# Optimization experiments

Hardware: AMD Instinct MI355X
Metric: run time of the kernel (lower is better)

Reference implementation:

```python
import jax, jax.numpy as jnp
import numpy as np

N, FEAT, H, D, E, C = 3072, 512, 8, 8, 100000, 2
ALPHA = 0.2  # LeakyReLU slope
NEG_INF = -9e15


def setup_inputs() -> dict:
    key = jax.random.key(0)
    ks = jax.random.split(key, 12)
    x = jax.random.normal(ks[0], (N, FEAT), dtype=jnp.float32)
    adj = (jax.random.uniform(ks[1], (N, N)) < 0.002).astype(jnp.float32)
    adj = jnp.maximum(adj, jnp.eye(N, dtype=jnp.float32))
    L = jax.random.randint(ks[2], (E,), 0, N)
    R = jax.random.randint(ks[3], (E,), 0, N)
    label = jax.random.randint(ks[4], (E,), 0, C)
    s = 1.0 / np.sqrt(FEAT)
    W = jax.random.uniform(ks[5], (H, FEAT, D), minval=-s, maxval=s, dtype=jnp.float32)
    sa = 1.0 / np.sqrt(2 * D)
    a1 = jax.random.uniform(ks[6], (H, D), minval=-sa, maxval=sa, dtype=jnp.float32)
    a2 = jax.random.uniform(ks[7], (H, D), minval=-sa, maxval=sa, dtype=jnp.float32)
    s1 = 1.0 / np.sqrt(H * D * 2)
    W1 = jax.random.uniform(ks[8], (H * D * 2, 64), minval=-s1, maxval=s1, dtype=jnp.float32)
    b1 = jnp.zeros((64,), dtype=jnp.float32)
    s2 = 1.0 / np.sqrt(64)
    W2 = jax.random.uniform(ks[9], (64, C), minval=-s2, maxval=s2, dtype=jnp.float32)
    b2 = jnp.zeros((C,), dtype=jnp.float32)
    return {"x": x, "adj": adj, "L": L, "R": R, "label": label,
            "W": W, "a1": a1, "a2": a2, "W1": W1, "b1": b1, "W2": W2, "b2": b2}


def _encoder(x, adj, W, a1, a2):
    # Wh: [H, N, D]
    Wh = jnp.einsum('nf,hfd->hnd', x, W)
    # broadcast attention logits: e[h,i,j] = leaky_relu(Wh_i.a1 + Wh_j.a2)
    s1 = jnp.einsum('hnd,hd->hn', Wh, a1)[:, :, None]   # [H,N,1]
    s2 = jnp.einsum('hnd,hd->hn', Wh, a2)[:, None, :]   # [H,1,N]
    e = jax.nn.leaky_relu(s1 + s2, negative_slope=ALPHA)  # [H,N,N]
    e = jnp.where(adj[None] > 0, e, NEG_INF)
    att = jax.nn.softmax(e, axis=-1)                      # [H,N,N]
    h = jnp.einsum('hnm,hmd->hnd', att, Wh)               # [H,N,D]
    h = jax.nn.elu(h)                                     # concat=True -> ELU
    # concat heads: [N, H*D]
    return jnp.transpose(h, (1, 0, 2)).reshape(x.shape[0], -1)


def reference(x, adj, L, R, label, W, a1, a2, W1, b1, W2, b2):
    emb = _encoder(x, adj, W, a1, a2)            # [N, 64]
    lr = jnp.concatenate([emb[L], emb[R]], axis=1)  # [E, 128]
    hcls = jax.nn.relu(lr @ W1 + b1)
    logits = hcls @ W2 + b2                       # [E, C]
    logp = jax.nn.log_softmax(logits, axis=-1)
    nll = -jnp.take_along_axis(logp, label[:, None], axis=1)[:, 0]
    return jnp.mean(nll)
```

## Files before the change

kernel.cpp:

```cpp
#include <hip/hip_runtime.h>
#include <math.h>

#define NN 3072
#define FEAT 512
#define HD 64
#define NE 100000
#define ALPHA 0.2f
#define CAP 96
#define CAPP 97
#define AROWS 8
#define K5_BLOCKS 2048

__global__ __launch_bounds__(256) void k_stage1(const float* __restrict__ adj, const float* __restrict__ x,
                                                const float* __restrict__ W, const float* __restrict__ a1,
                                                const float* __restrict__ a2, int* __restrict__ nbr,
                                                int* __restrict__ cnt, float* __restrict__ Wh,
                                                float* __restrict__ s1t, float* __restrict__ s2t) {
    __shared__ float xs4t[FEAT][4];
    __shared__ float part[4][4][HD];
    int b = blockIdx.x;
    int tid = threadIdx.x;
    int wid = tid >> 6, lane = tid & 63;

    if (b & 1) {
        int i = (b >> 1) * 4 + wid;
        const float4* row = (const float4*)&adj[(size_t)i * NN];
        float4 v[12];
        #pragma unroll
        for (int c = 0; c < 12; ++c) v[c] = row[c * 64 + lane];
        unsigned long long lmask = (1ull << lane) - 1ull;
        int base = 0;
        #pragma unroll
        for (int c = 0; c < 12; ++c) {
            #pragma unroll
            for (int k = 0; k < 4; ++k) {
                float vk = k == 0 ? v[c].x : k == 1 ? v[c].y : k == 2 ? v[c].z : v[c].w;
                bool nz = vk > 0.f;
                unsigned long long m = __ballot(nz);
                if (nz) {
                    int pos = base + __popcll(m & lmask);
                    if (pos < CAP) nbr[i * CAP + pos] = c * 256 + lane * 4 + k;
                }
                base += __popcll(m);
            }
        }
        if (lane == 0) cnt[i] = base < CAP ? base : CAP;
    } else {
        int n0 = (b >> 1) * 4;
        for (int idx = tid; idx < 512; idx += 256) {
            int r = idx >> 7, fq = idx & 127;
            float4 xv = ((const float4*)x)[(size_t)(n0 + r) * (FEAT / 4) + fq];
            xs4t[fq * 4 + 0][r] = xv.x;
            xs4t[fq * 4 + 1][r] = xv.y;
            xs4t[fq * 4 + 2][r] = xv.z;
            xs4t[fq * 4 + 3][r] = xv.w;
        }
        __syncthreads();
        int fsub = lane >> 4, h = (lane >> 1) & 7, dq = lane & 1;
        const float4* W4 = (const float4*)W;
        int base4 = h * 1024 + dq;
        int f0 = wid * (FEAT / 4);
        float4 acc0 = {0.f,0.f,0.f,0.f}, acc1 = acc0, acc2 = acc0, acc3 = acc0;
        #pragma unroll 8
        for (int f4 = 0; f4 < 32; ++f4) {
            int f = f0 + f4 * 4 + fsub;
            float4 w4 = W4[base4 + f * 2];
            float4 xv = *(const float4*)&xs4t[f][0];
            acc0.x = fmaf(xv.x, w4.x, acc0.x); acc0.y = fmaf(xv.x, w4.y, acc0.y);
            acc0.z = fmaf(xv.x, w4.z, acc0.z); acc0.w = fmaf(xv.x, w4.w, acc0.w);
            acc1.x = fmaf(xv.y, w4.x, acc1.x); acc1.y = fmaf(xv.y, w4.y, acc1.y);
            acc1.z = fmaf(xv.y, w4.z, acc1.z); acc1.w = fmaf(xv.y, w4.w, acc1.w);
            acc2.x = fmaf(xv.z, w4.x, acc2.x); acc2.y = fmaf(xv.z, w4.y, acc2.y);
            acc2.z = fmaf(xv.z, w4.z, acc2.z); acc2.w = fmaf(xv.z, w4.w, acc2.w);
            acc3.x = fmaf(xv.w, w4.x, acc3.x); acc3.y = fmaf(xv.w, w4.y, acc3.y);
            acc3.z = fmaf(xv.w, w4.z, acc3.z); acc3.w = fmaf(xv.w, w4.w, acc3.w);
        }
        #define RED4(A) \
            A.x += __shfl_xor(A.x, 16, 64); A.x += __shfl_xor(A.x, 32, 64); \
            A.y += __shfl_xor(A.y, 16, 64); A.y += __shfl_xor(A.y, 32, 64); \
            A.z += __shfl_xor(A.z, 16, 64); A.z += __shfl_xor(A.z, 32, 64); \
            A.w += __shfl_xor(A.w, 16, 64); A.w += __shfl_xor(A.w, 32, 64);
        RED4(acc0) RED4(acc1) RED4(acc2) RED4(acc3)
        #undef RED4
        if (fsub == 0) {
            int o = h * 8 + dq * 4;
            *(float4*)&part[wid][0][o] = acc0;
            *(float4*)&part[wid][1][o] = acc1;
            *(float4*)&part[wid][2][o] = acc2;
            *(float4*)&part[wid][3][o] = acc3;
        }
        __syncthreads();
        int n = n0 + wid;
        float v = part[0][wid][lane] + part[1][wid][lane] + part[2][wid][lane] + part[3][wid][lane];
        Wh[n * HD + lane] = v;
        float t1 = v * a1[lane];
        float t2 = v * a2[lane];
        for (int m = 1; m < 8; m <<= 1) {
            t1 += __shfl_xor(t1, m, 64);
            t2 += __shfl_xor(t2, m, 64);
        }
        if ((lane & 7) == 0) {
            int h2 = lane >> 3;
            s1t[n * 8 + h2] = t1;
            s2t[n * 8 + h2] = t2;
        }
    }
}

__global__ __launch_bounds__(512) void k_attn_pq(const float* __restrict__ Wh, const float* __restrict__ s1t,
                                                 const float* __restrict__ s2t, const int* __restrict__ nbr,
                                                 const int* __restrict__ cnt, const float* __restrict__ W1,
                                                 const float* __restrict__ b1, float* __restrict__ P,
                                                 float* __restrict__ Q) {
    __shared__ float W1s[2 * HD][HD];
    __shared__ int   jbuf[AROWS][CAP];
    __shared__ float ebuf[AROWS][8][CAPP];
    __shared__ float es[AROWS][HD];
    int tid = threadIdx.x;
    int wid = tid >> 6;
    int lane = tid & 63;
    int i = blockIdx.x * AROWS + wid;
    int h = lane >> 3, d = lane & 7;
    int ni = cnt[i];
    float s1i = s1t[i * 8 + h];
    for (int k = lane; k < CAP; k += 64)
        if (k < ni) jbuf[wid][k] = nbr[i * CAP + k];
    for (int idx = tid; idx < 2048; idx += 512)
        ((float4*)W1s)[idx] = ((const float4*)W1)[idx];
    __syncthreads();
    float mloc = -INFINITY;
    for (int k = d; k < ni; k += 8) {
        int j = jbuf[wid][k];
        float ev = s1i + s2t[j * 8 + h];
        ev = ev > 0.f ? ev : ALPHA * ev;
        ebuf[wid][h][k] = ev;
        mloc = fmaxf(mloc, ev);
    }
    mloc = fmaxf(mloc, __shfl_xor(mloc, 1, 8));
    mloc = fmaxf(mloc, __shfl_xor(mloc, 2, 8));
    mloc = fmaxf(mloc, __shfl_xor(mloc, 4, 8));
    __syncthreads();
    float denom = 0.f, acc = 0.f;
    for (int k = 0; k < ni; ++k) {
        float p = __expf(ebuf[wid][h][k] - mloc);
        denom += p;
        acc = fmaf(p, Wh[jbuf[wid][k] * HD + lane], acc);
    }
    float o = acc / denom;
    o = o > 0.f ? o : expm1f(o);
    es[wid][lane] = o;
    __syncthreads();
    float p = b1[lane], q = 0.f;
    #pragma unroll 8
    for (int k = 0; k < HD; ++k) {
        float e = es[wid][k];
        p = fmaf(e, W1s[k][lane], p);
        q = fmaf(e, W1s[HD + k][lane], q);
    }
    P[i * HD + lane] = p;
    Q[i * HD + lane] = q;
}

__global__ __launch_bounds__(256) void k_cls(const float* __restrict__ P, const float* __restrict__ Q,
                                             const int* __restrict__ L, const int* __restrict__ R,
                                             const int* __restrict__ label, const float* __restrict__ W2,
                                             const float* __restrict__ b2, float* __restrict__ partials) {
    int tid = threadIdx.x;
    int sl = tid & 15;
    int g = (blockIdx.x * 256 + tid) >> 4;
    float2 wa = *(const float2*)&W2[(sl * 4 + 0) * 2];
    float2 wb = *(const float2*)&W2[(sl * 4 + 1) * 2];
    float2 wc = *(const float2*)&W2[(sl * 4 + 2) * 2];
    float2 wd = *(const float2*)&W2[(sl * 4 + 3) * 2];
    float b20 = b2[0], b21 = b2[1];

    int e0 = g, e1 = g + 32768, e2 = g + 65536;
    int ln0 = L[e0], rn0 = R[e0], lb0 = label[e0];
    int ln1 = L[e1], rn1 = R[e1], lb1 = label[e1];
    int ln2 = L[e2], rn2 = R[e2], lb2 = label[e2];
    float4 p0 = *(const float4*)&P[ln0 * HD + sl * 4];
    float4 q0 = *(const float4*)&Q[rn0 * HD + sl * 4];
    float4 p1 = *(const float4*)&P[ln1 * HD + sl * 4];
    float4 q1 = *(const float4*)&Q[rn1 * HD + sl * 4];
    float4 p2 = *(const float4*)&P[ln2 * HD + sl * 4];
    float4 q2 = *(const float4*)&Q[rn2 * HD + sl * 4];

    float v00 = fmaxf(p0.x + q0.x, 0.f), v01 = fmaxf(p0.y + q0.y, 0.f);
    float v02 = fmaxf(p0.z + q0.z, 0.f), v03 = fmaxf(p0.w + q0.w, 0.f);
    float v10 = fmaxf(p1.x + q1.x, 0.f), v11 = fmaxf(p1.y + q1.y, 0.f);
    float v12 = fmaxf(p1.z + q1.z, 0.f), v13 = fmaxf(p1.w + q1.w, 0.f);
    float v20 = fmaxf(p2.x + q2.x, 0.f), v21 = fmaxf(p2.y + q2.y, 0.f);
    float v22 = fmaxf(p2.z + q2.z, 0.f), v23 = fmaxf(p2.w + q2.w, 0.f);

    float t00 = v00 * wa.x + v01 * wb.x + v02 * wc.x + v03 * wd.x;
    float t01 = v00 * wa.y + v01 * wb.y + v02 * wc.y + v03 * wd.y;
    float t10 = v10 * wa.x + v11 * wb.x + v12 * wc.x + v13 * wd.x;
    float t11 = v10 * wa.y + v11 * wb.y + v12 * wc.y + v13 * wd.y;
    float t20 = v20 * wa.x + v21 * wb.x + v22 * wc.x + v23 * wd.x;
    float t21 = v20 * wa.y + v21 * wb.y + v22 * wc.y + v23 * wd.y;
    #pragma unroll
    for (int m = 1; m < 16; m <<= 1) {
        t00 += __shfl_xor(t00, m, 64);  t01 += __shfl_xor(t01, m, 64);
        t10 += __shfl_xor(t10, m, 64);  t11 += __shfl_xor(t11, m, 64);
        t20 += __shfl_xor(t20, m, 64);  t21 += __shfl_xor(t21, m, 64);
    }
    float sum;
    {
        float l0 = t00 + b20, l1 = t01 + b21;
        float mx = fmaxf(l0, l1);
        sum = mx + __logf(__expf(l0 - mx) + __expf(l1 - mx)) - (lb0 ? l1 : l0);
        l0 = t10 + b20; l1 = t11 + b21; mx = fmaxf(l0, l1);
        sum += mx + __logf(__expf(l0 - mx) + __expf(l1 - mx)) - (lb1 ? l1 : l0);
        l0 = t20 + b20; l1 = t21 + b21; mx = fmaxf(l0, l1);
        sum += mx + __logf(__expf(l0 - mx) + __expf(l1 - mx)) - (lb2 ? l1 : l0);
    }
    if (g + 98304 < NE) {
        int e3 = g + 98304;
        int ln3 = L[e3], rn3 = R[e3], lb3 = label[e3];
        float4 p3 = *(const float4*)&P[ln3 * HD + sl * 4];
        float4 q3 = *(const float4*)&Q[rn3 * HD + sl * 4];
        float w0 = fmaxf(p3.x + q3.x, 0.f), w1 = fmaxf(p3.y + q3.y, 0.f);
        float w2 = fmaxf(p3.z + q3.z, 0.f), w3 = fmaxf(p3.w + q3.w, 0.f);
        float t30 = w0 * wa.x + w1 * wb.x + w2 * wc.x + w3 * wd.x;
        float t31 = w0 * wa.y + w1 * wb.y + w2 * wc.y + w3 * wd.y;
        #pragma unroll
        for (int m = 1; m < 16; m <<= 1) {
            t30 += __shfl_xor(t30, m, 64);  t31 += __shfl_xor(t31, m, 64);
        }
        float l0 = t30 + b20, l1 = t31 + b21;
        float mx = fmaxf(l0, l1);
        sum += mx + __logf(__expf(l0 - mx) + __expf(l1 - mx)) - (lb3 ? l1 : l0);
    }
    sum = (sl == 0) ? sum : 0.f;
    #pragma unroll
    for (int m = 1; m < 64; m <<= 1) sum += __shfl_xor(sum, m, 64);
    __shared__ float wsum[4];
    if ((tid & 63) == 0) wsum[tid >> 6] = sum;
    __syncthreads();
    if (tid == 0) partials[blockIdx.x] = wsum[0] + wsum[1] + wsum[2] + wsum[3];
}

__global__ __launch_bounds__(1024) void k_reduce(const float* __restrict__ partials, float* __restrict__ out) {
    __shared__ float sh[1024];
    int t = threadIdx.x;
    sh[t] = partials[t] + partials[t + 1024];
    __syncthreads();
    for (int s = 512; s > 0; s >>= 1) {
        if (t < s) sh[t] += sh[t + s];
        __syncthreads();
    }
    if (t == 0) out[0] = sh[0] / (float)NE;
}

extern "C" void kernel_launch(void* const* d_in, const int* in_sizes, int n_in,
                              void* d_out, int out_size, void* d_ws, size_t ws_size,
                              hipStream_t stream) {
    const float* x     = (const float*)d_in[0];
    const float* adj   = (const float*)d_in[1];
    const int*   L     = (const int*)d_in[2];
    const int*   R     = (const int*)d_in[3];
    const int*   label = (const int*)d_in[4];
    const float* W     = (const float*)d_in[5];
    const float* a1    = (const float*)d_in[6];
    const float* a2    = (const float*)d_in[7];
    const float* W1    = (const float*)d_in[8];
    const float* b1    = (const float*)d_in[9];
    const float* W2    = (const float*)d_in[10];
    const float* b2    = (const float*)d_in[11];

    char* ws = (char*)d_ws;
    float* Wh       = (float*)(ws + 0);
    float* s1t      = (float*)(ws + 786432);
    float* s2t      = (float*)(ws + 884736);
    int*   cnt      = (int*)  (ws + 983040);
    int*   nbr      = (int*)  (ws + 995328);
    float* P        = (float*)(ws + 2174976);
    float* Q        = (float*)(ws + 2961408);
    float* partials = (float*)(ws + 3747840);

    k_stage1<<<2 * (NN / 4), 256, 0, stream>>>(adj, x, W, a1, a2, nbr, cnt, Wh, s1t, s2t);
    k_attn_pq<<<NN / AROWS, 512, 0, stream>>>(Wh, s1t, s2t, nbr, cnt, W1, b1, P, Q);
    k_cls<<<K5_BLOCKS, 256, 0, stream>>>(P, Q, L, R, label, W2, b2, partials);
    k_reduce<<<1, 1024, 0, stream>>>(partials, (float*)d_out);
}
```

Before: 39.19 us.

## Split adjacency compaction across four waves per row and restructure x staging

Each adjacency row is now compacted by a whole 256-thread block: four waves each scan a quarter of the row, publish their popcounts through shared memory, and write neighbour indices at prefix offsets. This replaces one wave per row with 12 serial ballot chunks, increasing parallelism and shortening the per-wave dependency chain for the dominant adjacency read. The Wh blocks are moved to the front of the grid, x is staged row-major with float4 stores instead of a transposed scatter, and the loop unroll drops from 8 to 4. It adds a block barrier and more blocks (3072 row blocks instead of 768), and x reads in the inner loop become four scalar LDS loads instead of one float4.

```diff
diff --git a/kernel.cpp b/kernel.cpp
--- a/kernel.cpp
+++ b/kernel.cpp
@@ -9,6 +9,7 @@
 #define CAP 96
 #define CAPP 97
 #define AROWS 8
+#define WH_BLOCKS 768
 #define K5_BLOCKS 2048
 
 __global__ __launch_bounds__(256) void k_stage1(const float* __restrict__ adj, const float* __restrict__ x,
@@ -16,44 +17,58 @@
                                                 const float* __restrict__ a2, int* __restrict__ nbr,
                                                 int* __restrict__ cnt, float* __restrict__ Wh,
                                                 float* __restrict__ s1t, float* __restrict__ s2t) {
-    __shared__ float xs4t[FEAT][4];
+    __shared__ float xs[4][FEAT];
     __shared__ float part[4][4][HD];
+    __shared__ int   wcnt[4];
     int b = blockIdx.x;
     int tid = threadIdx.x;
     int wid = tid >> 6, lane = tid & 63;
 
-    if (b & 1) {
-        int i = (b >> 1) * 4 + wid;
-        const float4* row = (const float4*)&adj[(size_t)i * NN];
-        float4 v[12];
-        #pragma unroll
-        for (int c = 0; c < 12; ++c) v[c] = row[c * 64 + lane];
+    if (b >= WH_BLOCKS) {
+        int i = b - WH_BLOCKS;
+        const float4* row4 = (const float4*)&adj[(size_t)i * NN];
+        float4 v[3];
+        #pragma unroll
+        for (int c = 0; c < 3; ++c) v[c] = row4[wid * 192 + c * 64 + lane];
         unsigned long long lmask = (1ull << lane) - 1ull;
-        int base = 0;
-        #pragma unroll
-        for (int c = 0; c < 12; ++c) {
+        int wc = 0;
+        unsigned long long masks[12];
+        #pragma unroll
+        for (int c = 0; c < 3; ++c) {
             #pragma unroll
             for (int k = 0; k < 4; ++k) {
                 float vk = k == 0 ? v[c].x : k == 1 ? v[c].y : k == 2 ? v[c].z : v[c].w;
-                bool nz = vk > 0.f;
-                unsigned long long m = __ballot(nz);
-                if (nz) {
+                unsigned long long m = __ballot(vk > 0.f);
+                masks[c * 4 + k] = m;
+                wc += __popcll(m);
+            }
+        }
+        if (lane == 0) wcnt[wid] = wc;
+        __syncthreads();
+        int base = 0;
+        #pragma unroll
+        for (int w2 = 0; w2 < 4; ++w2) if (w2 < wid) base += wcnt[w2];
+        #pragma unroll
+        for (int c = 0; c < 3; ++c) {
+            #pragma unroll
+            for (int k = 0; k < 4; ++k) {
+                unsigned long long m = masks[c * 4 + k];
+                if ((m >> lane) & 1ull) {
                     int pos = base + __popcll(m & lmask);
-                    if (pos < CAP) nbr[i * CAP + pos] = c * 256 + lane * 4 + k;
+                    if (pos < CAP) nbr[i * CAP + pos] = wid * 768 + c * 256 + lane * 4 + k;
                 }
                 base += __popcll(m);
             }
         }
-        if (lane == 0) cnt[i] = base < CAP ? base : CAP;
+        if (tid == 0) {
+            int tot = wcnt[0] + wcnt[1] + wcnt[2] + wcnt[3];
+            cnt[i] = tot < CAP ? tot : CAP;
+        }
     } else {
-        int n0 = (b >> 1) * 4;
+        int n0 = b * 4;
         for (int idx = tid; idx < 512; idx += 256) {
             int r = idx >> 7, fq = idx & 127;
-            float4 xv = ((const float4*)x)[(size_t)(n0 + r) * (FEAT / 4) + fq];
-            xs4t[fq * 4 + 0][r] = xv.x;
-            xs4t[fq * 4 + 1][r] = xv.y;
-            xs4t[fq * 4 + 2][r] = xv.z;
-            xs4t[fq * 4 + 3][r] = xv.w;
+            *(float4*)&xs[r][fq * 4] = ((const float4*)x)[(size_t)(n0 + r) * (FEAT / 4) + fq];
         }
         __syncthreads();
         int fsub = lane >> 4, h = (lane >> 1) & 7, dq = lane & 1;
@@ -61,19 +76,19 @@
         int base4 = h * 1024 + dq;
         int f0 = wid * (FEAT / 4);
         float4 acc0 = {0.f,0.f,0.f,0.f}, acc1 = acc0, acc2 = acc0, acc3 = acc0;
-        #pragma unroll 8
+        #pragma unroll 4
         for (int f4 = 0; f4 < 32; ++f4) {
             int f = f0 + f4 * 4 + fsub;
             float4 w4 = W4[base4 + f * 2];
-            float4 xv = *(const float4*)&xs4t[f][0];
-            acc0.x = fmaf(xv.x, w4.x, acc0.x); acc0.y = fmaf(xv.x, w4.y, acc0.y);
-            acc0.z = fmaf(xv.x, w4.z, acc0.z); acc0.w = fmaf(xv.x, w4.w, acc0.w);
-            acc1.x = fmaf(xv.y, w4.x, acc1.x); acc1.y = fmaf(xv.y, w4.y, acc1.y);
-            acc1.z = fmaf(xv.y, w4.z, acc1.z); acc1.w = fmaf(xv.y, w4.w, acc1.w);
-            acc2.x = fmaf(xv.z, w4.x, acc2.x); acc2.y = fmaf(xv.z, w4.y, acc2.y);
-            acc2.z = fmaf(xv.z, w4.z, acc2.z); acc2.w = fmaf(xv.z, w4.w, acc2.w);
-            acc3.x = fmaf(xv.w, w4.x, acc3.x); acc3.y = fmaf(xv.w, w4.y, acc3.y);
-            acc3.z = fmaf(xv.w, w4.z, acc3.z); acc3.w = fmaf(xv.w, w4.w, acc3.w);
+            float x0 = xs[0][f], x1 = xs[1][f], x2 = xs[2][f], x3 = xs[3][f];
+            acc0.x = fmaf(x0, w4.x, acc0.x); acc0.y = fmaf(x0, w4.y, acc0.y);
+            acc0.z = fmaf(x0, w4.z, acc0.z); acc0.w = fmaf(x0, w4.w, acc0.w);
+            acc1.x = fmaf(x1, w4.x, acc1.x); acc1.y = fmaf(x1, w4.y, acc1.y);
+            acc1.z = fmaf(x1, w4.z, acc1.z); acc1.w = fmaf(x1, w4.w, acc1.w);
+            acc2.x = fmaf(x2, w4.x, acc2.x); acc2.y = fmaf(x2, w4.y, acc2.y);
+            acc2.z = fmaf(x2, w4.z, acc2.z); acc2.w = fmaf(x2, w4.w, acc2.w);
+            acc3.x = fmaf(x3, w4.x, acc3.x); acc3.y = fmaf(x3, w4.y, acc3.y);
+            acc3.z = fmaf(x3, w4.z, acc3.z); acc3.w = fmaf(x3, w4.w, acc3.w);
         }
         #define RED4(A) \
             A.x += __shfl_xor(A.x, 16, 64); A.x += __shfl_xor(A.x, 32, 64); \
@@ -278,7 +293,7 @@
     float* Q        = (float*)(ws + 2961408);
     float* partials = (float*)(ws + 3747840);
 
-    k_stage1<<<2 * (NN / 4), 256, 0, stream>>>(adj, x, W, a1, a2, nbr, cnt, Wh, s1t, s2t);
+    k_stage1<<<WH_BLOCKS + NN, 256, 0, stream>>>(adj, x, W, a1, a2, nbr, cnt, Wh, s1t, s2t);
     k_attn_pq<<<NN / AROWS, 512, 0, stream>>>(Wh, s1t, s2t, nbr, cnt, W1, b1, P, Q);
     k_cls<<<K5_BLOCKS, 256, 0, stream>>>(P, Q, L, R, label, W2, b2, partials);
     k_reduce<<<1, 1024, 0, stream>>>(partials, (float*)d_out);
```

New measurement: 34.55 us (median of 2 runs). 11.8% less time.
